# Kernel tuning notes

Measured on AMD Instinct MI355X. Metric: run time of the kernel, lower is better.

The kernel has to match this reference:

```python
import jax, jax.numpy as jnp
import numpy as np


def conv1x1(x, w, b):
    # x: [B,Cin,H,W], w: [Cout,Cin], b: [Cout]
    return jnp.einsum('bchw,oc->bohw', x, w) + b[None, :, None, None]


def setup_inputs() -> dict:
    key = jax.random.key(0)
    ks = jax.random.split(key, 10)
    B, Cm, C, H, W = 4, 6, 64, 64, 64
    map1 = jax.random.normal(ks[0], (B, Cm, H, W), jnp.float32)
    map2 = jax.random.normal(ks[1], (B, Cm, H, W), jnp.float32)
    feature_map = jax.random.normal(ks[2], (B, C, H, W), jnp.float32)
    # 1x1 conv params (kaiming-ish scale)
    wb = jax.random.normal(ks[3], (Cm, Cm), jnp.float32) / np.sqrt(Cm)
    bb = jnp.zeros((Cm,), jnp.float32)
    wc = jax.random.normal(ks[4], (Cm, Cm), jnp.float32) / np.sqrt(Cm)
    bc = jnp.zeros((Cm,), jnp.float32)
    wd = jax.random.normal(ks[5], (C, C), jnp.float32) / np.sqrt(C)
    bd = jnp.zeros((C,), jnp.float32)
    alpha = jnp.zeros((1,), jnp.float32)
    return {"map1": map1, "map2": map2, "feature_map": feature_map,
            "wb": wb, "bb": bb, "wc": wc, "bc": bc, "wd": wd, "bd": bd,
            "alpha": alpha}


def reference(map1, map2, feature_map, wb, bb, wc, bc, wd, bd, alpha):
    B, _, H, W = map1.shape
    N = H * W
    # conv1x1 projections, flatten spatial
    feat_b = conv1x1(map1, wb, bb).reshape(B, -1, N).transpose(0, 2, 1)  # [B,N,6]
    feat_c = conv1x1(map2, wc, bc).reshape(B, -1, N)                      # [B,6,N]
    attention_s = jax.nn.softmax(jnp.einsum('bnc,bcm->bnm', feat_b, feat_c), axis=-1)  # [B,N,N]
    feat_d = conv1x1(feature_map, wd, bd).reshape(B, -1, N)               # [B,C,N]
    # bmm with attention_s^T: out[b,c,n] = sum_m feat_d[b,c,m] * attn[b,n,m]
    feat_e = jnp.einsum('bcm,bnm->bcn', feat_d, attention_s).reshape(B, -1, H, W)
    return alpha * feat_e + feature_map
```

## Files before the change

kernel.cpp:

```cpp
#include <hip/hip_runtime.h>
#include <hip/hip_bf16.h>
#include <math.h>


#define BATCH 4
#define CMAP  6
#define CH    64
#define NSP   4096
#define TN    64
#define NTQ   16

typedef __attribute__((ext_vector_type(8))) short short8;
typedef __attribute__((ext_vector_type(4))) float f32x4;

#if __has_builtin(__builtin_amdgcn_exp2f)
#define EXP2(x) __builtin_amdgcn_exp2f(x)
#else
#define EXP2(x) exp2f(x)
#endif

__device__ __forceinline__ unsigned f2bf(float f) {
    unsigned u = __float_as_uint(f);
    return (u + 0x7fffu + ((u >> 16) & 1u)) >> 16;
}
__device__ __forceinline__ unsigned char f2fp8(float f) {
    return (unsigned char)(__builtin_amdgcn_cvt_pk_fp8_f32(f, f, 0u, false) & 0xffu);
}

#define INVLN2 1.44269504088896f
#define SHIFT_BF16 0xC238u
#define ONE_BF16   0x3F80u


__global__ void proj_kernel(const float* __restrict__ map1, const float* __restrict__ map2,
                            const float* __restrict__ fm,
                            const float* __restrict__ wb, const float* __restrict__ bb,
                            const float* __restrict__ wc, const float* __restrict__ bc,
                            const float* __restrict__ wd, const float* __restrict__ bd,
                            unsigned short* __restrict__ featq8,
                            unsigned short* __restrict__ featk8,
                            unsigned char* __restrict__ featdf)
{
    __shared__ unsigned char vfrag[2048];

    const int b    = blockIdx.z;
    const int half = blockIdx.y;
    const int lane = threadIdx.x & 63;
    const int og   = threadIdx.x >> 6;
    const int n    = blockIdx.x * 64 + lane;

    const int ht = lane >> 5;
    const int mm = lane & 31;
    const int q4 = mm >> 3, jj = mm & 7;
    const int cb_local = og >> 1;
    float vals[CH];
#pragma unroll
    for (int c = 0; c < CH; ++c)
        vals[c] = fm[(size_t)(b*CH + c)*NSP + n];
#pragma unroll
    for (int oi = 0; oi < 8; ++oi) {
        const int o = half*32 + og*8 + oi;
        float a = bd[o];
#pragma unroll
        for (int c = 0; c < CH; ++c)
            a = fmaf(vals[c], wd[o*CH + c], a);
        const int r = (og & 1)*8 + oi;
        vfrag[(ht*2 + cb_local)*512 + (q4*16 + r)*8 + jj] = f2fp8(a);
    }

    if (half == 0 && og == 0) {
        float v1[CMAP], v2[CMAP];
#pragma unroll
        for (int c = 0; c < CMAP; ++c) {
            v1[c] = map1[(size_t)(b*CMAP + c)*NSP + n];
            v2[c] = map2[(size_t)(b*CMAP + c)*NSP + n];
        }
        unsigned qv[CMAP], kv[CMAP];
#pragma unroll
        for (int o = 0; o < CMAP; ++o) {
            float a1 = bb[o], a2 = bc[o];
#pragma unroll
            for (int c = 0; c < CMAP; ++c) {
                a1 = fmaf(v1[c], wb[o*CMAP + c], a1);
                a2 = fmaf(v2[c], wc[o*CMAP + c], a2);
            }
            qv[o] = f2bf(a1 * INVLN2);
            kv[o] = f2bf(a2);
        }
        uint4 qw, kw;
        qw.x = qv[0] | (qv[1] << 16);
        qw.y = qv[2] | (qv[3] << 16);
        qw.z = qv[4] | (qv[5] << 16);
        qw.w = SHIFT_BF16;
        kw.x = kv[0] | (kv[1] << 16);
        kw.y = kv[2] | (kv[3] << 16);
        kw.z = kv[4] | (kv[5] << 16);
        kw.w = ONE_BF16;
        *(uint4*)&featq8[(size_t)(b*NSP + n)*8] = qw;
        *(uint4*)&featk8[(size_t)(b*NSP + n)*8] = kw;
    }

    __syncthreads();

    {
        const int tt = threadIdx.x;
        const uint2 d = *(const uint2*)&vfrag[tt*8];
        const int ht2 = tt >> 7, inner = tt & 127;
        const size_t off = (((size_t)(b*128 + blockIdx.x*2 + ht2)*4) + half*2)*512
                         + (size_t)inner*8;
        *(uint2*)&featdf[off] = d;
    }
}

__global__ __launch_bounds__(256, 2)
void attn_kernel(const unsigned short* __restrict__ featq8,
                 const unsigned short* __restrict__ featk8,
                 const unsigned char* __restrict__ featdf,
                 const float* __restrict__ fm, const float* __restrict__ alpha_p,
                 float* __restrict__ out)
{
    __shared__ float cmb[3][64][36];

    const int b    = blockIdx.y;
    const int t    = threadIdx.x;
    const int lane = t & 63, w = t >> 6;
    const int row16 = lane & 15, quad = lane >> 4;
    const int n0   = blockIdx.x * 32;
    const int m0   = w * (NSP/4);

    short8 qf0 = {0,0,0,0,0,0,0,0}, qf1 = {0,0,0,0,0,0,0,0};
    if (quad == 0) {
        qf0 = *(const short8*)&featq8[(size_t)(b*NSP + n0 + row16)*8];
        qf1 = *(const short8*)&featq8[(size_t)(b*NSP + n0 + 16 + row16)*8];
    }

    const long long onesA = 0x3838383838383838LL;

    const int perm16 = ((row16 >> 2) << 3) + (row16 & 3);
    const unsigned short* kbase = featk8 + ((size_t)(b*NSP + m0) + perm16)*8 + quad*8;
    const unsigned char* vfb = featdf + ((size_t)b*128*4)*512 + lane*8;
    const int hb = w * 32;

    const f32x4 zf = {0.f,0.f,0.f,0.f};
    f32x4 acc[8] = {zf,zf,zf,zf,zf,zf,zf,zf};
    f32x4 accL2[2] = {zf, zf};
    f32x4 sp[8];
    short8 kc[4];
    long long vv[8], pb[4];

#define LOADK(mt)                                                               \
    kc[0] = *(const short8*)(kbase + ((mt)*TN +  0)*8);                         \
    kc[1] = *(const short8*)(kbase + ((mt)*TN +  4)*8);                         \
    kc[2] = *(const short8*)(kbase + ((mt)*TN + 32)*8);                         \
    kc[3] = *(const short8*)(kbase + ((mt)*TN + 36)*8);

#define LOADV(vt)                                                               \
    _Pragma("unroll")                                                           \
    for (int cb = 0; cb < 4; ++cb) {                                            \
        vv[cb*2+0] = *(const long long*)(vfb + (size_t)((hb + (vt)*2 + 0)*4 + cb)*512); \
        vv[cb*2+1] = *(const long long*)(vfb + (size_t)((hb + (vt)*2 + 1)*4 + cb)*512); \
    }

#define SCORES(dst)                                                             \
    _Pragma("unroll")                                                           \
    for (int kr = 0; kr < 4; ++kr) {                                            \
        dst[kr]   = __builtin_amdgcn_mfma_f32_16x16x32_bf16(kc[kr], qf0, zf, 0, 0, 0); \
        dst[4+kr] = __builtin_amdgcn_mfma_f32_16x16x32_bf16(kc[kr], qf1, zf, 0, 0, 0); \
    }

#define EXPPACK(g)                                                              \
    {                                                                           \
        float e[16];                                                            \
        _Pragma("unroll")                                                       \
        for (int u = 0; u < 4; ++u) {                                           \
            e[u*4+0] = EXP2(sp[(g)*4+u][0]);                                    \
            e[u*4+1] = EXP2(sp[(g)*4+u][1]);                                    \
            e[u*4+2] = EXP2(sp[(g)*4+u][2]);                                    \
            e[u*4+3] = EXP2(sp[(g)*4+u][3]);                                    \
        }                                                                       \
        unsigned lo0 = __builtin_amdgcn_cvt_pk_fp8_f32(e[0],  e[1],  0u,  false); \
        lo0          = __builtin_amdgcn_cvt_pk_fp8_f32(e[2],  e[3],  lo0, true);  \
        unsigned hi0 = __builtin_amdgcn_cvt_pk_fp8_f32(e[4],  e[5],  0u,  false); \
        hi0          = __builtin_amdgcn_cvt_pk_fp8_f32(e[6],  e[7],  hi0, true);  \
        unsigned lo1 = __builtin_amdgcn_cvt_pk_fp8_f32(e[8],  e[9],  0u,  false); \
        lo1          = __builtin_amdgcn_cvt_pk_fp8_f32(e[10], e[11], lo1, true);  \
        unsigned hi1 = __builtin_amdgcn_cvt_pk_fp8_f32(e[12], e[13], 0u,  false); \
        hi1          = __builtin_amdgcn_cvt_pk_fp8_f32(e[14], e[15], hi1, true);  \
        pb[(g)*2+0] = (long long)(((unsigned long long)hi0 << 32) | lo0);       \
        pb[(g)*2+1] = (long long)(((unsigned long long)hi1 << 32) | lo1);       \
    }

#define PVALL                                                                   \
    _Pragma("unroll")                                                           \
    for (int g = 0; g < 2; ++g) {                                               \
        _Pragma("unroll")                                                       \
        for (int cb = 0; cb < 4; ++cb) {                                        \
            acc[g*4+cb] = __builtin_amdgcn_mfma_f32_16x16x32_fp8_fp8(vv[cb*2+0], pb[g*2+0], acc[g*4+cb], 0, 0, 0); \
            acc[g*4+cb] = __builtin_amdgcn_mfma_f32_16x16x32_fp8_fp8(vv[cb*2+1], pb[g*2+1], acc[g*4+cb], 0, 0, 0); \
        }                                                                       \
        accL2[g] = __builtin_amdgcn_mfma_f32_16x16x32_fp8_fp8(onesA, pb[g*2+0], accL2[g], 0, 0, 0); \
        accL2[g] = __builtin_amdgcn_mfma_f32_16x16x32_fp8_fp8(onesA, pb[g*2+1], accL2[g], 0, 0, 0); \
    }

    LOADK(0)
    SCORES(sp)
    LOADK(1)
    LOADV(0)

    for (int i = 1; i < NTQ; ++i) {
        f32x4 tt2[8];
        SCORES(tt2)
        LOADK(i + 1)

        EXPPACK(0)
        EXPPACK(1)
        PVALL

        LOADV(i)
#pragma unroll
        for (int u = 0; u < 8; ++u) sp[u] = tt2[u];
    }

    EXPPACK(0)
    EXPPACK(1)
    PVALL
#undef LOADK
#undef LOADV
#undef SCORES
#undef EXPPACK
#undef PVALL

    if (w != 0) {
        float* c = cmb[w - 1][lane];
#pragma unroll
        for (int i = 0; i < 8; ++i)
            *(float4*)&c[i*4] = (float4){acc[i][0], acc[i][1], acc[i][2], acc[i][3]};
        c[32] = accL2[0][0];
        c[33] = accL2[1][0];
    }
    __syncthreads();
    if (w == 0) {
        float l0 = accL2[0][0], l1 = accL2[1][0];
#pragma unroll
        for (int ww = 0; ww < 3; ++ww) {
            const float* c = cmb[ww][lane];
#pragma unroll
            for (int i = 0; i < 8; ++i) {
                const float4 po = *(const float4*)&c[i*4];
                acc[i][0] += po.x; acc[i][1] += po.y;
                acc[i][2] += po.z; acc[i][3] += po.w;
            }
            l0 += c[32];
            l1 += c[33];
        }
        const float alpha = alpha_p[0];
        const float cinv[2] = { alpha / (l0 + 1e-30f), alpha / (l1 + 1e-30f) };
#pragma unroll
        for (int g = 0; g < 2; ++g) {
            const int n = n0 + g*16 + row16;
#pragma unroll
            for (int cb = 0; cb < 4; ++cb) {
#pragma unroll
                for (int r = 0; r < 4; ++r) {
                    const int ch = cb*16 + quad*4 + r;
                    const size_t idx = (size_t)(b*CH + ch)*NSP + n;
                    out[idx] = fmaf(cinv[g], acc[g*4+cb][r], fm[idx]);
                }
            }
        }
    }
}

extern "C" void kernel_launch(void* const* d_in, const int* in_sizes, int n_in,
                              void* d_out, int out_size, void* d_ws, size_t ws_size,
                              hipStream_t stream)
{
    const float* map1  = (const float*)d_in[0];
    const float* map2  = (const float*)d_in[1];
    const float* fm    = (const float*)d_in[2];
    const float* wb    = (const float*)d_in[3];
    const float* bb    = (const float*)d_in[4];
    const float* wc    = (const float*)d_in[5];
    const float* bc    = (const float*)d_in[6];
    const float* wd    = (const float*)d_in[7];
    const float* bd    = (const float*)d_in[8];
    const float* alpha = (const float*)d_in[9];
    float* out = (float*)d_out;

    unsigned short* featq8 = (unsigned short*)d_ws;
    unsigned short* featk8 = featq8 + (size_t)BATCH*NSP*8;
    unsigned char*  featdf = (unsigned char*)(featk8 + (size_t)BATCH*NSP*8);

    proj_kernel<<<dim3(NSP/64, 2, BATCH), 256, 0, stream>>>(
        map1, map2, fm, wb, bb, wc, bc, wd, bd, featq8, featk8, featdf);
    attn_kernel<<<dim3(NSP/32, BATCH), 256, 0, stream>>>(
        featq8, featk8, featdf, fm, alpha, out);
}
```

Before: 108.0 us.

## Pre-swizzle K and V into per-lane fragment layout for wide contiguous loads

```diff
diff --git a/kernel.cpp b/kernel.cpp
--- a/kernel.cpp
+++ b/kernel.cpp
@@ -12,6 +12,7 @@
 
 typedef __attribute__((ext_vector_type(8))) short short8;
 typedef __attribute__((ext_vector_type(4))) float f32x4;
+typedef __attribute__((ext_vector_type(2))) long long ll2;
 
 #if __has_builtin(__builtin_amdgcn_exp2f)
 #define EXP2(x) __builtin_amdgcn_exp2f(x)
@@ -38,10 +39,11 @@
                             const float* __restrict__ wc, const float* __restrict__ bc,
                             const float* __restrict__ wd, const float* __restrict__ bd,
                             unsigned short* __restrict__ featq8,
-                            unsigned short* __restrict__ featk8,
-                            unsigned char* __restrict__ featdf)
+                            unsigned short* __restrict__ featkf,
+                            unsigned char* __restrict__ featvf)
 {
     __shared__ unsigned char vfrag[2048];
+    __shared__ unsigned short kq[64*8];
 
     const int b    = blockIdx.z;
     const int half = blockIdx.y;
@@ -97,25 +99,35 @@
         kw.z = kv[4] | (kv[5] << 16);
         kw.w = ONE_BF16;
         *(uint4*)&featq8[(size_t)(b*NSP + n)*8] = qw;
-        *(uint4*)&featk8[(size_t)(b*NSP + n)*8] = kw;
+        *(uint4*)&kq[lane*8] = kw;
     }
 
     __syncthreads();
 
-    {
-        const int tt = threadIdx.x;
-        const uint2 d = *(const uint2*)&vfrag[tt*8];
-        const int ht2 = tt >> 7, inner = tt & 127;
-        const size_t off = (((size_t)(b*128 + blockIdx.x*2 + ht2)*4) + half*2)*512
-                         + (size_t)inner*8;
-        *(uint2*)&featdf[off] = d;
+    if (threadIdx.x < 128) {
+        const int l  = threadIdx.x & 63;
+        const int h2 = threadIdx.x >> 6;
+        const uint2 a0 = *(const uint2*)&vfrag[(h2*2 + 0)*512 + l*8];
+        const uint2 a1 = *(const uint2*)&vfrag[(h2*2 + 1)*512 + l*8];
+        uint4 d; d.x = a0.x; d.y = a0.y; d.z = a1.x; d.w = a1.y;
+        *(uint4*)&featvf[(((size_t)(b*64 + blockIdx.x))*64 + l)*64 + h2*32 + half*16] = d;
+    }
+
+    if (half == 0) {
+        const int s = threadIdx.x >> 6, l = threadIdx.x & 63;
+        uint4 d = {0u, 0u, 0u, 0u};
+        if (l < 16) {
+            const int row = (((l >> 2) << 3) + (l & 3)) + (s & 1)*4 + (s >> 1)*32;
+            d = *(const uint4*)&kq[row*8];
+        }
+        *(uint4*)&featkf[(((size_t)(b*64 + blockIdx.x)*4 + s)*64 + l)*8] = d;
     }
 }
 
 __global__ __launch_bounds__(256, 2)
 void attn_kernel(const unsigned short* __restrict__ featq8,
-                 const unsigned short* __restrict__ featk8,
-                 const unsigned char* __restrict__ featdf,
+                 const unsigned short* __restrict__ featkf,
+                 const unsigned char* __restrict__ featvf,
                  const float* __restrict__ fm, const float* __restrict__ alpha_p,
                  float* __restrict__ out)
 {
@@ -126,7 +138,6 @@
     const int lane = t & 63, w = t >> 6;
     const int row16 = lane & 15, quad = lane >> 4;
     const int n0   = blockIdx.x * 32;
-    const int m0   = w * (NSP/4);
 
     short8 qf0 = {0,0,0,0,0,0,0,0}, qf1 = {0,0,0,0,0,0,0,0};
     if (quad == 0) {
@@ -136,29 +147,31 @@
 
     const long long onesA = 0x3838383838383838LL;
 
-    const int perm16 = ((row16 >> 2) << 3) + (row16 & 3);
-    const unsigned short* kbase = featk8 + ((size_t)(b*NSP + m0) + perm16)*8 + quad*8;
-    const unsigned char* vfb = featdf + ((size_t)b*128*4)*512 + lane*8;
-    const int hb = w * 32;
+    const unsigned short* kb0 = featkf + ((size_t)(b*64 + w*16)*4)*64*8 + lane*8;
+    const unsigned char*  vb0 = featvf + ((size_t)(b*64 + w*16))*4096 + lane*64;
 
     const f32x4 zf = {0.f,0.f,0.f,0.f};
     f32x4 acc[8] = {zf,zf,zf,zf,zf,zf,zf,zf};
     f32x4 accL2[2] = {zf, zf};
     f32x4 sp[8];
     short8 kc[4];
-    long long vv[8], pb[4];
+    ll2 vq[4];
+    long long pb[4];
 
 #define LOADK(mt)                                                               \
-    kc[0] = *(const short8*)(kbase + ((mt)*TN +  0)*8);                         \
-    kc[1] = *(const short8*)(kbase + ((mt)*TN +  4)*8);                         \
-    kc[2] = *(const short8*)(kbase + ((mt)*TN + 32)*8);                         \
-    kc[3] = *(const short8*)(kbase + ((mt)*TN + 36)*8);
+    {   const unsigned short* kp = kb0 + (size_t)(mt)*2048;                     \
+        kc[0] = *(const short8*)(kp);                                           \
+        kc[1] = *(const short8*)(kp + 512);                                     \
+        kc[2] = *(const short8*)(kp + 1024);                                    \
+        kc[3] = *(const short8*)(kp + 1536);                                    \
+    }
 
 #define LOADV(vt)                                                               \
-    _Pragma("unroll")                                                           \
-    for (int cb = 0; cb < 4; ++cb) {                                            \
-        vv[cb*2+0] = *(const long long*)(vfb + (size_t)((hb + (vt)*2 + 0)*4 + cb)*512); \
-        vv[cb*2+1] = *(const long long*)(vfb + (size_t)((hb + (vt)*2 + 1)*4 + cb)*512); \
+    {   const unsigned char* vp = vb0 + (size_t)(vt)*4096;                      \
+        vq[0] = *(const ll2*)(vp);                                              \
+        vq[1] = *(const ll2*)(vp + 16);                                         \
+        vq[2] = *(const ll2*)(vp + 32);                                         \
+        vq[3] = *(const ll2*)(vp + 48);                                         \
     }
 
 #define SCORES(dst)                                                             \
@@ -195,8 +208,8 @@
     for (int g = 0; g < 2; ++g) {                                               \
         _Pragma("unroll")                                                       \
         for (int cb = 0; cb < 4; ++cb) {                                        \
-            acc[g*4+cb] = __builtin_amdgcn_mfma_f32_16x16x32_fp8_fp8(vv[cb*2+0], pb[g*2+0], acc[g*4+cb], 0, 0, 0); \
-            acc[g*4+cb] = __builtin_amdgcn_mfma_f32_16x16x32_fp8_fp8(vv[cb*2+1], pb[g*2+1], acc[g*4+cb], 0, 0, 0); \
+            acc[g*4+cb] = __builtin_amdgcn_mfma_f32_16x16x32_fp8_fp8(vq[(cb>>1)][cb&1],     pb[g*2+0], acc[g*4+cb], 0, 0, 0); \
+            acc[g*4+cb] = __builtin_amdgcn_mfma_f32_16x16x32_fp8_fp8(vq[2 + (cb>>1)][cb&1], pb[g*2+1], acc[g*4+cb], 0, 0, 0); \
         }                                                                       \
         accL2[g] = __builtin_amdgcn_mfma_f32_16x16x32_fp8_fp8(onesA, pb[g*2+0], accL2[g], 0, 0, 0); \
         accL2[g] = __builtin_amdgcn_mfma_f32_16x16x32_fp8_fp8(onesA, pb[g*2+1], accL2[g], 0, 0, 0); \
@@ -210,7 +223,7 @@
     for (int i = 1; i < NTQ; ++i) {
         f32x4 tt2[8];
         SCORES(tt2)
-        LOADK(i + 1)
+        LOADK((i + 1) & 15)
 
         EXPPACK(0)
         EXPPACK(1)
@@ -288,11 +301,11 @@
     float* out = (float*)d_out;
 
     unsigned short* featq8 = (unsigned short*)d_ws;
-    unsigned short* featk8 = featq8 + (size_t)BATCH*NSP*8;
-    unsigned char*  featdf = (unsigned char*)(featk8 + (size_t)BATCH*NSP*8);
+    unsigned short* featkf = featq8 + (size_t)BATCH*NSP*8;
+    unsigned char*  featvf = (unsigned char*)(featkf + (size_t)BATCH*64*4*64*8);
 
     proj_kernel<<<dim3(NSP/64, 2, BATCH), 256, 0, stream>>>(
-        map1, map2, fm, wb, bb, wc, bc, wd, bd, featq8, featk8, featdf);
+        map1, map2, fm, wb, bb, wc, bc, wd, bd, featq8, featkf, featvf);
     attn_kernel<<<dim3(NSP/32, BATCH), 256, 0, stream>>>(
-        featq8, featk8, featdf, fm, alpha, out);
-}
+        featq8, featkf, featvf, fm, alpha, out);
+}
```

Result: no change. 106.1 us (-1.8%).
